# Performance work log

Hardware: AMD Instinct MI355X
Metric: run time of the kernel (lower is better)

The kernel has to match this reference:

```python
import jax, jax.numpy as jnp
import numpy as np

B, S, D_IN, D_EMB = 8, 2048, 512, 512

def setup_inputs() -> dict:
    key = jax.random.key(0)
    ks = jax.random.split(key, 7)
    s = 1.0 / np.sqrt(D_IN)
    return {
        "x": jax.random.normal(ks[0], (B, S, D_IN), dtype=jnp.float32),
        "Wq": jax.random.uniform(ks[1], (D_IN, D_EMB), jnp.float32, -s, s),
        "bq": jax.random.uniform(ks[2], (D_EMB,), jnp.float32, -s, s),
        "Wk": jax.random.uniform(ks[3], (D_IN, D_EMB), jnp.float32, -s, s),
        "bk": jax.random.uniform(ks[4], (D_EMB,), jnp.float32, -s, s),
        "Wv": jax.random.uniform(ks[5], (D_IN, D_EMB), jnp.float32, -s, s),
        "bv": jax.random.uniform(ks[6], (D_EMB,), jnp.float32, -s, s),
    }

def reference(x, Wq, bq, Wk, bk, Wv, bv):
    # single-head attention: softmax(QK^T / sqrt(d)) V
    q = x @ Wq + bq            # [B,S,E]
    k = x @ Wk + bk
    v = x @ Wv + bv
    scores = jnp.einsum('bse,bte->bst', q, k) / jnp.sqrt(jnp.float32(D_EMB))
    attn = jax.nn.softmax(scores, axis=-1)  # [B,S,S]
    return jnp.einsum('bst,bte->bse', attn, v)
```

## Files before the change

kernel.cpp:

```cpp
#include <hip/hip_runtime.h>
#include <stdint.h>


using f32x4 = __attribute__((ext_vector_type(4))) float;
using s16x8 = __attribute__((ext_vector_type(8))) short;
using u16x4 = __attribute__((ext_vector_type(4))) unsigned short;

#define S_LEN 2048
#define EMB   512

#define ASYNC16(g, l)                                                     \
  __builtin_amdgcn_global_load_lds(                                       \
      (const __attribute__((address_space(1))) void*)(g),                 \
      (__attribute__((address_space(3))) void*)(l), 16, 0, 0)

__device__ __forceinline__ unsigned short f2bf(float f) {
  union { float f; unsigned u; } v; v.f = f;
  unsigned r = v.u + 0x7fffu + ((v.u >> 16) & 1u);
  return (unsigned short)(r >> 16);
}

__global__ __launch_bounds__(256) void xconv_kernel(
    const float* __restrict__ x, short* __restrict__ xb) {
  int i = (blockIdx.x * 256 + threadIdx.x) * 8;
  f32x4 a = *(const f32x4*)(x + i);
  f32x4 b = *(const f32x4*)(x + i + 4);
  s16x8 h;
  h[0] = (short)f2bf(a[0]); h[1] = (short)f2bf(a[1]);
  h[2] = (short)f2bf(a[2]); h[3] = (short)f2bf(a[3]);
  h[4] = (short)f2bf(b[0]); h[5] = (short)f2bf(b[1]);
  h[6] = (short)f2bf(b[2]); h[7] = (short)f2bf(b[3]);
  *(s16x8*)(xb + i) = h;
}

__global__ __launch_bounds__(256) void wconv_kernel(
    const float* __restrict__ Wq, const float* __restrict__ Wk,
    const float* __restrict__ Wv, short* __restrict__ Wt) {
  __shared__ float T[64][65];
  int bid = blockIdx.x;
  int mat = bid >> 6;
  int t   = bid & 63;
  int k0  = (t & 7) << 6, n0 = (t >> 3) << 6;
  const float* W = (mat == 0) ? Wq : (mat == 1) ? Wk : Wv;
  int tid = threadIdx.x;
  int rr = tid >> 4, cc = tid & 15;
#pragma unroll
  for (int p = 0; p < 4; ++p) {
    int row = p * 16 + rr;
    f32x4 v = *(const f32x4*)(W + (size_t)(k0 + row) * 512 + n0 + cc * 4);
#pragma unroll
    for (int j = 0; j < 4; ++j) T[row][cc * 4 + j] = v[j];
  }
  __syncthreads();
  short* D = Wt + (size_t)mat * 262144;
#pragma unroll
  for (int p = 0; p < 4; ++p) {
    int nrow = p * 16 + rr;
    u16x4 h;
#pragma unroll
    for (int j = 0; j < 4; ++j) h[j] = f2bf(T[cc * 4 + j][nrow]);
    *(u16x4*)(D + (size_t)(n0 + nrow) * 512 + k0 + cc * 4) = h;
  }
}

__global__ __launch_bounds__(256) void qkv_gemm(
    const short* __restrict__ xb, const short* __restrict__ Wt,
    const float* __restrict__ bq, const float* __restrict__ bk,
    const float* __restrict__ bv,
    short* __restrict__ Qg, short* __restrict__ Kg, short* __restrict__ VTg) {
  __shared__ __align__(16) short As[2][128 * 64];
  __shared__ __align__(16) short Bs[2][128 * 64];
  int gid = blockIdx.x;
  int xcd = gid & 7;
  int s   = gid >> 3;
  int mt_l = s / 12;
  int j    = s - mt_l * 12;
  int mat  = j >> 2;
  int nt   = j & 3;
  int mt   = xcd * 16 + mt_l;
  int m0   = mt << 7, n0 = nt << 7;
  const short* W    = Wt + (size_t)mat * 262144;
  const float* bias = (mat == 0) ? bq : (mat == 1) ? bk : bv;

  int tid = threadIdx.x, lane = tid & 63, wv = tid >> 6;
  int l16 = lane & 15, quad = lane >> 4;
  int wr = (wv & 1) << 6, wc = (wv >> 1) << 6;
  int drow = lane >> 3;
  int dchk = (lane & 7) ^ drow;

  const short* asrc[4];
  const short* bsrc[4];
#pragma unroll
  for (int i = 0; i < 4; ++i) {
    int row = (wv * 4 + i) * 8 + drow;
    asrc[i] = xb + (size_t)(m0 + row) * 512 + dchk * 8;
    bsrc[i] = W  + (size_t)(n0 + row) * 512 + dchk * 8;
  }

  const f32x4 Z4 = {0.f, 0.f, 0.f, 0.f};
  f32x4 acc[4][4];
#pragma unroll
  for (int a = 0; a < 4; ++a)
#pragma unroll
    for (int c = 0; c < 4; ++c) acc[a][c] = Z4;

#pragma unroll
  for (int i = 0; i < 4; ++i) {
    int g = wv * 4 + i;
    ASYNC16(asrc[i], &As[0][g * 512]);
    ASYNC16(bsrc[i], &Bs[0][g * 512]);
  }
  __syncthreads();

  for (int it = 0; it < 8; ++it) {
    int buf = it & 1;
    if (it < 7) {
      int k1 = (it + 1) << 6;
#pragma unroll
      for (int i = 0; i < 4; ++i) {
        int g = wv * 4 + i;
        ASYNC16(asrc[i] + k1, &As[buf ^ 1][g * 512]);
        ASYNC16(bsrc[i] + k1, &Bs[buf ^ 1][g * 512]);
      }
    }
#pragma unroll
    for (int kk = 0; kk < 2; ++kk) {
      s16x8 af[4], bfr[4];
#pragma unroll
      for (int rb = 0; rb < 4; ++rb) {
        int row = wr + rb * 16 + l16;
        int c   = kk * 4 + quad;
        af[rb] = *(const s16x8*)(&As[buf][row * 64 + ((c ^ (row & 7)) * 8)]);
      }
#pragma unroll
      for (int cb = 0; cb < 4; ++cb) {
        int row = wc + cb * 16 + l16;
        int c   = kk * 4 + quad;
        bfr[cb] = *(const s16x8*)(&Bs[buf][row * 64 + ((c ^ (row & 7)) * 8)]);
      }
#pragma unroll
      for (int rb = 0; rb < 4; ++rb)
#pragma unroll
        for (int cb = 0; cb < 4; ++cb)
          acc[rb][cb] = __builtin_amdgcn_mfma_f32_16x16x32_bf16(af[rb], bfr[cb], acc[rb][cb], 0, 0, 0);
    }
    __syncthreads();
  }

  float bsv[4];
#pragma unroll
  for (int cb = 0; cb < 4; ++cb) bsv[cb] = bias[n0 + wc + cb * 16 + l16];

  if (mat < 2) {
    short* D  = (mat == 0) ? Qg : Kg;
    short* Ct = &As[0][0];
#pragma unroll
    for (int rb = 0; rb < 4; ++rb)
#pragma unroll
      for (int cb = 0; cb < 4; ++cb)
#pragma unroll
        for (int r = 0; r < 4; ++r) {
          int m_l = wr + rb * 16 + quad * 4 + r;
          int e_l = wc + cb * 16 + l16;
          int cc  = e_l >> 3;
          Ct[m_l * 128 + ((cc ^ (m_l & 7)) * 8) + (e_l & 7)] =
              (short)f2bf(acc[rb][cb][r] + bsv[cb]);
        }
    __syncthreads();
#pragma unroll
    for (int g = 0; g < 8; ++g) {
      int row = wv * 32 + g * 4 + (lane >> 4);
      int cc  = lane & 15;
      s16x8 v = *(const s16x8*)(Ct + row * 128 + ((cc ^ (row & 7)) * 8));
      *(s16x8*)(D + (size_t)(m0 + row) * 512 + n0 + cc * 8) = v;
    }
  } else {
#pragma unroll
    for (int rb = 0; rb < 4; ++rb)
#pragma unroll
      for (int cb = 0; cb < 4; ++cb) {
        u16x4 h;
#pragma unroll
        for (int r = 0; r < 4; ++r) h[r] = f2bf(acc[rb][cb][r] + bsv[cb]);
        int m  = m0 + wr + rb * 16 + quad * 4;
        int bb = m >> 11, sl = m & 2047;
        int e  = n0 + wc + cb * 16 + l16;
        size_t idx = ((((size_t)bb * 32 + (e >> 4)) * 64 + (sl >> 5)) * 16 +
                      (e & 15)) * 32 + (sl & 31);
        *(u16x4*)(VTg + idx) = h;
      }
  }
}

__global__ __launch_bounds__(512, 2) void attn_kernel(
    const short* __restrict__ Qg, const short* __restrict__ Kg,
    const short* __restrict__ VTg, float* __restrict__ out) {
  __shared__ __align__(16) short Kt[3][32 * 512];
  __shared__ __align__(16) short Pl[2][64 * 40];
  __shared__ float l_l[64];
  const float SCL2 = 0.06375871855f;

  int b = blockIdx.x & 7, qt = blockIdx.x >> 3;
  int s0 = qt << 6;
  int rot = (qt << 1) & 63;
  int tid = threadIdx.x, lane = tid & 63, wv = tid >> 6;
  int l16 = lane & 15, quad = lane >> 4;

  const short* Kb = Kg  + (size_t)b * S_LEN * 512;
  const short* Vb = VTg + (size_t)b * 1048576;

  const short* kdma[4];
#pragma unroll
  for (int i = 0; i < 4; ++i) {
    int r = wv * 4 + i;
    kdma[i] = Kb + (size_t)r * 512 + ((lane ^ (r & 7)) * 8);
  }

  {
    size_t a0 = (size_t)rot * 16384;
    size_t a1 = (size_t)((rot + 1) & 63) * 16384;
#pragma unroll
    for (int i = 0; i < 4; ++i)
      ASYNC16(kdma[i] + a0, &Kt[0][(wv * 4 + i) * 512]);
#pragma unroll
    for (int i = 0; i < 4; ++i)
      ASYNC16(kdma[i] + a1, &Kt[1][(wv * 4 + i) * 512]);
  }

  if (wv < 4) {
    int a = wv & 1, h = wv >> 1;
    const short* qrowA = Qg + ((size_t)b * S_LEN + s0 + a * 32 + l16) * 512 + quad * 8;
    const short* qrowB = qrowA + (size_t)16 * 512;
    s16x8 qfA[16], qfB[16];
#pragma unroll
    for (int c = 0; c < 16; ++c) {
      qfA[c] = *(const s16x8*)(qrowA + c * 32);
      qfB[c] = *(const s16x8*)(qrowB + c * 32);
    }
    const f32x4 Z4 = {0.f, 0.f, 0.f, 0.f};
    f32x4 lsumA = Z4, lsumB = Z4;

    __syncthreads();

    for (int kt = 0; kt < 64; ++kt) {
      int rbuf = kt % 3, wbuf = (kt + 2) % 3;
      {
        size_t adv = (size_t)((kt + 2 + rot) & 63) * 16384;
#pragma unroll
        for (int i = 0; i < 4; ++i)
          ASYNC16(kdma[i] + adv, &Kt[wbuf][(wv * 4 + i) * 512]);
      }
      __builtin_amdgcn_sched_barrier(0);

      f32x4 sA = Z4, sB = Z4;
      int krow = h * 16 + l16;
      const short* kb = &Kt[rbuf][krow * 512];
      int ksw = krow & 7;
      __builtin_amdgcn_s_setprio(1);
#pragma unroll
      for (int c = 0; c < 16; ++c) {
        s16x8 kf = *(const s16x8*)(kb + (((c * 4 + quad) ^ ksw) * 8));
        sA = __builtin_amdgcn_mfma_f32_16x16x32_bf16(qfA[c], kf, sA, 0, 0, 0);
        sB = __builtin_amdgcn_mfma_f32_16x16x32_bf16(qfB[c], kf, sB, 0, 0, 0);
      }
      __builtin_amdgcn_s_setprio(0);

      short* Pc = Pl[kt & 1];
#pragma unroll
      for (int r = 0; r < 4; ++r) {
        float pA = exp2f(sA[r] * SCL2);
        lsumA[r] += pA;
        Pc[(a * 32 + quad * 4 + r) * 40 + h * 16 + l16] = (short)f2bf(pA);
        float pB = exp2f(sB[r] * SCL2);
        lsumB[r] += pB;
        Pc[(a * 32 + 16 + quad * 4 + r) * 40 + h * 16 + l16] = (short)f2bf(pB);
      }

      asm volatile("s_waitcnt vmcnt(4) lgkmcnt(0)\n\ts_barrier" ::: "memory");
      __builtin_amdgcn_sched_barrier(0);
    }

#pragma unroll
    for (int r = 0; r < 4; ++r) {
      float vA = lsumA[r];
      vA += __shfl_xor(vA, 1); vA += __shfl_xor(vA, 2);
      vA += __shfl_xor(vA, 4); vA += __shfl_xor(vA, 8);
      lsumA[r] = vA;
      float vB = lsumB[r];
      vB += __shfl_xor(vB, 1); vB += __shfl_xor(vB, 2);
      vB += __shfl_xor(vB, 4); vB += __shfl_xor(vB, 8);
      lsumB[r] = vB;
    }
    if (h == 0 && l16 == 0) {
#pragma unroll
      for (int r = 0; r < 4; ++r) {
        l_l[a * 32 + quad * 4 + r]      = lsumA[r];
        l_l[a * 32 + 16 + quad * 4 + r] = lsumB[r];
      }
    }
    __syncthreads();
    if (h == 1 && l16 == 0) {
#pragma unroll
      for (int r = 0; r < 4; ++r) {
        l_l[a * 32 + quad * 4 + r]      += lsumA[r];
        l_l[a * 32 + 16 + quad * 4 + r] += lsumB[r];
      }
    }
    __syncthreads();
  } else {
    int pw = wv - 4;
    int e0 = pw << 7;
    const short* vbase = Vb + (size_t)pw * 262144 + l16 * 32 + quad * 8;

    const f32x4 Z4 = {0.f, 0.f, 0.f, 0.f};
    f32x4 acc[4][8];
#pragma unroll
    for (int g = 0; g < 4; ++g)
#pragma unroll
      for (int cb = 0; cb < 8; ++cb) acc[g][cb] = Z4;
    s16x8 vfA[8], vfB[8];

    __syncthreads();

    for (int kt = 0; kt < 64; kt += 2) {
      {
        size_t adv = (size_t)((kt + 2 + rot) & 63) * 16384;
        int wbuf = (kt + 2) % 3;
#pragma unroll
        for (int i = 0; i < 4; ++i)
          ASYNC16(kdma[i] + adv, &Kt[wbuf][(wv * 4 + i) * 512]);
      }
      {
        size_t vadv = (size_t)((kt + rot) & 63) * 512;
#pragma unroll
        for (int cb = 0; cb < 8; ++cb)
          vfA[cb] = *(const s16x8*)(vbase + (size_t)cb * 32768 + vadv);
      }
      if (kt) {
        s16x8 pf[4];
#pragma unroll
        for (int g = 0; g < 4; ++g)
          pf[g] = *(const s16x8*)(&Pl[1][(g * 16 + l16) * 40 + quad * 8]);
        __builtin_amdgcn_s_setprio(1);
#pragma unroll
        for (int cb = 0; cb < 8; ++cb)
#pragma unroll
          for (int g = 0; g < 4; ++g)
            acc[g][cb] = __builtin_amdgcn_mfma_f32_16x16x32_bf16(pf[g], vfB[cb], acc[g][cb], 0, 0, 0);
        __builtin_amdgcn_s_setprio(0);
      }
      asm volatile("s_waitcnt lgkmcnt(0)\n\ts_barrier" ::: "memory");
      __builtin_amdgcn_sched_barrier(0);

      {
        size_t adv = (size_t)((kt + 3 + rot) & 63) * 16384;
        int wbuf = (kt + 3) % 3;
#pragma unroll
        for (int i = 0; i < 4; ++i)
          ASYNC16(kdma[i] + adv, &Kt[wbuf][(wv * 4 + i) * 512]);
      }
      {
        size_t vadv = (size_t)((kt + 1 + rot) & 63) * 512;
#pragma unroll
        for (int cb = 0; cb < 8; ++cb)
          vfB[cb] = *(const s16x8*)(vbase + (size_t)cb * 32768 + vadv);
      }
      {
        s16x8 pf[4];
#pragma unroll
        for (int g = 0; g < 4; ++g)
          pf[g] = *(const s16x8*)(&Pl[0][(g * 16 + l16) * 40 + quad * 8]);
        __builtin_amdgcn_s_setprio(1);
#pragma unroll
        for (int cb = 0; cb < 8; ++cb)
#pragma unroll
          for (int g = 0; g < 4; ++g)
            acc[g][cb] = __builtin_amdgcn_mfma_f32_16x16x32_bf16(pf[g], vfA[cb], acc[g][cb], 0, 0, 0);
        __builtin_amdgcn_s_setprio(0);
      }
      asm volatile("s_waitcnt lgkmcnt(0)\n\ts_barrier" ::: "memory");
      __builtin_amdgcn_sched_barrier(0);
    }

    asm volatile("s_waitcnt vmcnt(0)" ::: "memory");
    __builtin_amdgcn_sched_barrier(0);
    {
      s16x8 pf[4];
#pragma unroll
      for (int g = 0; g < 4; ++g)
        pf[g] = *(const s16x8*)(&Pl[1][(g * 16 + l16) * 40 + quad * 8]);
#pragma unroll
      for (int cb = 0; cb < 8; ++cb)
#pragma unroll
        for (int g = 0; g < 4; ++g)
          acc[g][cb] = __builtin_amdgcn_mfma_f32_16x16x32_bf16(pf[g], vfB[cb], acc[g][cb], 0, 0, 0);
    }
    __syncthreads();
    __syncthreads();

#pragma unroll
    for (int g = 0; g < 4; ++g) {
      f32x4 lv = *(const f32x4*)(l_l + g * 16 + quad * 4);
      f32x4 li;
#pragma unroll
      for (int r = 0; r < 4; ++r) li[r] = 1.0f / lv[r];
#pragma unroll
      for (int cb = 0; cb < 8; ++cb)
#pragma unroll
        for (int r = 0; r < 4; ++r)
          out[((size_t)b * S_LEN + s0 + g * 16 + quad * 4 + r) * 512 + e0 + cb * 16 + l16] =
              acc[g][cb][r] * li[r];
    }
  }
}

extern "C" void kernel_launch(void* const* d_in, const int* in_sizes, int n_in,
                              void* d_out, int out_size, void* d_ws, size_t ws_size,
                              hipStream_t stream) {
  const float* x  = (const float*)d_in[0];
  const float* Wq = (const float*)d_in[1];
  const float* bq = (const float*)d_in[2];
  const float* Wk = (const float*)d_in[3];
  const float* bk = (const float*)d_in[4];
  const float* Wv = (const float*)d_in[5];
  const float* bv = (const float*)d_in[6];

  short* Wt  = (short*)d_ws;
  short* xb  = (short*)((char*)d_ws + 1572864);
  short* Qg  = xb + (size_t)8388608;
  short* Kg  = Qg + (size_t)8388608;
  short* VTg = Kg + (size_t)8388608;

  xconv_kernel<<<4096, 256, 0, stream>>>(x, xb);
  wconv_kernel<<<192, 256, 0, stream>>>(Wq, Wk, Wv, Wt);
  qkv_gemm<<<1536, 256, 0, stream>>>(xb, Wt, bq, bk, bv, Qg, Kg, VTg);
  attn_kernel<<<256, 512, 0, stream>>>(Qg, Kg, VTg, (float*)d_out);
}
```

Before: 213.7 us.

## Merge conversion kernels and fuse QKV GEMM with attention via cooperative grid sync

```diff
diff --git a/kernel.cpp b/kernel.cpp
--- a/kernel.cpp
+++ b/kernel.cpp
@@ -1,5 +1,8 @@
 #include <hip/hip_runtime.h>
+#include <hip/hip_cooperative_groups.h>
 #include <stdint.h>
+
+namespace cg = cooperative_groups;
 
 
 using f32x4 = __attribute__((ext_vector_type(4))) float;
@@ -20,396 +23,413 @@
   return (unsigned short)(r >> 16);
 }
 
-__global__ __launch_bounds__(256) void xconv_kernel(
-    const float* __restrict__ x, short* __restrict__ xb) {
-  int i = (blockIdx.x * 256 + threadIdx.x) * 8;
-  f32x4 a = *(const f32x4*)(x + i);
-  f32x4 b = *(const f32x4*)(x + i + 4);
-  s16x8 h;
-  h[0] = (short)f2bf(a[0]); h[1] = (short)f2bf(a[1]);
-  h[2] = (short)f2bf(a[2]); h[3] = (short)f2bf(a[3]);
-  h[4] = (short)f2bf(b[0]); h[5] = (short)f2bf(b[1]);
-  h[6] = (short)f2bf(b[2]); h[7] = (short)f2bf(b[3]);
-  *(s16x8*)(xb + i) = h;
-}
-
-__global__ __launch_bounds__(256) void wconv_kernel(
+__global__ __launch_bounds__(256) void conv_kernel(
+    const float* __restrict__ x, short* __restrict__ xb,
     const float* __restrict__ Wq, const float* __restrict__ Wk,
     const float* __restrict__ Wv, short* __restrict__ Wt) {
   __shared__ float T[64][65];
-  int bid = blockIdx.x;
-  int mat = bid >> 6;
-  int t   = bid & 63;
-  int k0  = (t & 7) << 6, n0 = (t >> 3) << 6;
-  const float* W = (mat == 0) ? Wq : (mat == 1) ? Wk : Wv;
-  int tid = threadIdx.x;
-  int rr = tid >> 4, cc = tid & 15;
-#pragma unroll
-  for (int p = 0; p < 4; ++p) {
-    int row = p * 16 + rr;
-    f32x4 v = *(const f32x4*)(W + (size_t)(k0 + row) * 512 + n0 + cc * 4);
-#pragma unroll
-    for (int j = 0; j < 4; ++j) T[row][cc * 4 + j] = v[j];
-  }
-  __syncthreads();
-  short* D = Wt + (size_t)mat * 262144;
-#pragma unroll
-  for (int p = 0; p < 4; ++p) {
-    int nrow = p * 16 + rr;
-    u16x4 h;
-#pragma unroll
-    for (int j = 0; j < 4; ++j) h[j] = f2bf(T[cc * 4 + j][nrow]);
-    *(u16x4*)(D + (size_t)(n0 + nrow) * 512 + k0 + cc * 4) = h;
+  if (blockIdx.x < 4096) {
+    int i = (blockIdx.x * 256 + threadIdx.x) * 8;
+    f32x4 a = *(const f32x4*)(x + i);
+    f32x4 b = *(const f32x4*)(x + i + 4);
+    s16x8 h;
+    h[0] = (short)f2bf(a[0]); h[1] = (short)f2bf(a[1]);
+    h[2] = (short)f2bf(a[2]); h[3] = (short)f2bf(a[3]);
+    h[4] = (short)f2bf(b[0]); h[5] = (short)f2bf(b[1]);
+    h[6] = (short)f2bf(b[2]); h[7] = (short)f2bf(b[3]);
+    *(s16x8*)(xb + i) = h;
+  } else {
+    int bid = blockIdx.x - 4096;
+    int mat = bid >> 6;
+    int t   = bid & 63;
+    int k0  = (t & 7) << 6, n0 = (t >> 3) << 6;
+    const float* W = (mat == 0) ? Wq : (mat == 1) ? Wk : Wv;
+    int tid = threadIdx.x;
+    int rr = tid >> 4, cc = tid & 15;
+#pragma unroll
+    for (int p = 0; p < 4; ++p) {
+      int row = p * 16 + rr;
+      f32x4 v = *(const f32x4*)(W + (size_t)(k0 + row) * 512 + n0 + cc * 4);
+#pragma unroll
+      for (int j = 0; j < 4; ++j) T[row][cc * 4 + j] = v[j];
+    }
+    __syncthreads();
+    short* D = Wt + (size_t)mat * 262144;
+#pragma unroll
+    for (int p = 0; p < 4; ++p) {
+      int nrow = p * 16 + rr;
+      u16x4 h;
+#pragma unroll
+      for (int j = 0; j < 4; ++j) h[j] = f2bf(T[cc * 4 + j][nrow]);
+      *(u16x4*)(D + (size_t)(n0 + nrow) * 512 + k0 + cc * 4) = h;
+    }
   }
 }
 
-__global__ __launch_bounds__(256) void qkv_gemm(
+__global__ __launch_bounds__(512, 2) void mega_kernel(
     const short* __restrict__ xb, const short* __restrict__ Wt,
     const float* __restrict__ bq, const float* __restrict__ bk,
     const float* __restrict__ bv,
-    short* __restrict__ Qg, short* __restrict__ Kg, short* __restrict__ VTg) {
-  __shared__ __align__(16) short As[2][128 * 64];
-  __shared__ __align__(16) short Bs[2][128 * 64];
-  int gid = blockIdx.x;
-  int xcd = gid & 7;
-  int s   = gid >> 3;
-  int mt_l = s / 12;
-  int j    = s - mt_l * 12;
-  int mat  = j >> 2;
-  int nt   = j & 3;
-  int mt   = xcd * 16 + mt_l;
-  int m0   = mt << 7, n0 = nt << 7;
-  const short* W    = Wt + (size_t)mat * 262144;
-  const float* bias = (mat == 0) ? bq : (mat == 1) ? bk : bv;
-
-  int tid = threadIdx.x, lane = tid & 63, wv = tid >> 6;
-  int l16 = lane & 15, quad = lane >> 4;
-  int wr = (wv & 1) << 6, wc = (wv >> 1) << 6;
-  int drow = lane >> 3;
-  int dchk = (lane & 7) ^ drow;
-
-  const short* asrc[4];
-  const short* bsrc[4];
-#pragma unroll
-  for (int i = 0; i < 4; ++i) {
-    int row = (wv * 4 + i) * 8 + drow;
-    asrc[i] = xb + (size_t)(m0 + row) * 512 + dchk * 8;
-    bsrc[i] = W  + (size_t)(n0 + row) * 512 + dchk * 8;
-  }
-
-  const f32x4 Z4 = {0.f, 0.f, 0.f, 0.f};
-  f32x4 acc[4][4];
-#pragma unroll
-  for (int a = 0; a < 4; ++a)
-#pragma unroll
-    for (int c = 0; c < 4; ++c) acc[a][c] = Z4;
-
-#pragma unroll
-  for (int i = 0; i < 4; ++i) {
-    int g = wv * 4 + i;
-    ASYNC16(asrc[i], &As[0][g * 512]);
-    ASYNC16(bsrc[i], &Bs[0][g * 512]);
-  }
-  __syncthreads();
-
-  for (int it = 0; it < 8; ++it) {
-    int buf = it & 1;
-    if (it < 7) {
-      int k1 = (it + 1) << 6;
+    short* __restrict__ Qg, short* __restrict__ Kg, short* __restrict__ VTg,
+    float* __restrict__ out) {
+  __shared__ __align__(16) char SM[131072];
+  const float SCL2 = 0.06375871855f;
+
+  int blk = blockIdx.x, tid = threadIdx.x;
+  int lane512 = tid & 63;
+
+  {
+    int hh = tid >> 8;
+    int tl = tid & 255;
+    int lane = tl & 63, wv = tl >> 6;
+    int l16 = lane & 15, quad = lane >> 4;
+    int xcd = blk & 7;
+
+    short* As = (short*)(SM + hh * 65536);
+    short* Bs = (short*)(SM + hh * 65536 + 32768);
+
+    int wr = (wv & 1) << 6, wc = (wv >> 1) << 6;
+    int drow = lane >> 3;
+    int dchk = (lane & 7) ^ drow;
+    const f32x4 Z4 = {0.f, 0.f, 0.f, 0.f};
+
+    for (int job = 0; job < 3; ++job) {
+      int s    = (blk >> 3) * 6 + hh * 3 + job;
+      int mt_l = s / 12;
+      int jj   = s - mt_l * 12;
+      int mat  = jj >> 2;
+      int nt   = jj & 3;
+      int mt   = xcd * 16 + mt_l;
+      int m0   = mt << 7, n0 = nt << 7;
+      const short* W    = Wt + (size_t)mat * 262144;
+      const float* bias = (mat == 0) ? bq : (mat == 1) ? bk : bv;
+
+      const short* asrc[4];
+      const short* bsrc[4];
+#pragma unroll
+      for (int i = 0; i < 4; ++i) {
+        int row = (wv * 4 + i) * 8 + drow;
+        asrc[i] = xb + (size_t)(m0 + row) * 512 + dchk * 8;
+        bsrc[i] = W  + (size_t)(n0 + row) * 512 + dchk * 8;
+      }
+
+      f32x4 acc[4][4];
+#pragma unroll
+      for (int a = 0; a < 4; ++a)
+#pragma unroll
+        for (int c = 0; c < 4; ++c) acc[a][c] = Z4;
+
 #pragma unroll
       for (int i = 0; i < 4; ++i) {
         int g = wv * 4 + i;
-        ASYNC16(asrc[i] + k1, &As[buf ^ 1][g * 512]);
-        ASYNC16(bsrc[i] + k1, &Bs[buf ^ 1][g * 512]);
-      }
-    }
-#pragma unroll
-    for (int kk = 0; kk < 2; ++kk) {
-      s16x8 af[4], bfr[4];
-#pragma unroll
-      for (int rb = 0; rb < 4; ++rb) {
-        int row = wr + rb * 16 + l16;
-        int c   = kk * 4 + quad;
-        af[rb] = *(const s16x8*)(&As[buf][row * 64 + ((c ^ (row & 7)) * 8)]);
-      }
-#pragma unroll
-      for (int cb = 0; cb < 4; ++cb) {
-        int row = wc + cb * 16 + l16;
-        int c   = kk * 4 + quad;
-        bfr[cb] = *(const s16x8*)(&Bs[buf][row * 64 + ((c ^ (row & 7)) * 8)]);
-      }
-#pragma unroll
-      for (int rb = 0; rb < 4; ++rb)
-#pragma unroll
-        for (int cb = 0; cb < 4; ++cb)
-          acc[rb][cb] = __builtin_amdgcn_mfma_f32_16x16x32_bf16(af[rb], bfr[cb], acc[rb][cb], 0, 0, 0);
-    }
-    __syncthreads();
+        ASYNC16(asrc[i], As + g * 512);
+        ASYNC16(bsrc[i], Bs + g * 512);
+      }
+      __syncthreads();
+
+      for (int it = 0; it < 8; ++it) {
+        int buf = it & 1;
+        if (it < 7) {
+          int k1 = (it + 1) << 6;
+#pragma unroll
+          for (int i = 0; i < 4; ++i) {
+            int g = wv * 4 + i;
+            ASYNC16(asrc[i] + k1, As + (buf ^ 1) * 8192 + g * 512);
+            ASYNC16(bsrc[i] + k1, Bs + (buf ^ 1) * 8192 + g * 512);
+          }
+        }
+#pragma unroll
+        for (int kk = 0; kk < 2; ++kk) {
+          s16x8 af[4], bfr[4];
+#pragma unroll
+          for (int rb = 0; rb < 4; ++rb) {
+            int row = wr + rb * 16 + l16;
+            int c   = kk * 4 + quad;
+            af[rb] = *(const s16x8*)(As + buf * 8192 + row * 64 + ((c ^ (row & 7)) * 8));
+          }
+#pragma unroll
+          for (int cb = 0; cb < 4; ++cb) {
+            int row = wc + cb * 16 + l16;
+            int c   = kk * 4 + quad;
+            bfr[cb] = *(const s16x8*)(Bs + buf * 8192 + row * 64 + ((c ^ (row & 7)) * 8));
+          }
+#pragma unroll
+          for (int rb = 0; rb < 4; ++rb)
+#pragma unroll
+            for (int cb = 0; cb < 4; ++cb)
+              acc[rb][cb] = __builtin_amdgcn_mfma_f32_16x16x32_bf16(af[rb], bfr[cb], acc[rb][cb], 0, 0, 0);
+        }
+        __syncthreads();
+      }
+
+      float bsv[4];
+#pragma unroll
+      for (int cb = 0; cb < 4; ++cb) bsv[cb] = bias[n0 + wc + cb * 16 + l16];
+
+      if (mat < 2) {
+        short* D  = (mat == 0) ? Qg : Kg;
+        short* Ct = As;
+#pragma unroll
+        for (int rb = 0; rb < 4; ++rb)
+#pragma unroll
+          for (int cb = 0; cb < 4; ++cb)
+#pragma unroll
+            for (int r = 0; r < 4; ++r) {
+              int m_l = wr + rb * 16 + quad * 4 + r;
+              int e_l = wc + cb * 16 + l16;
+              int cc  = e_l >> 3;
+              Ct[m_l * 128 + ((cc ^ (m_l & 7)) * 8) + (e_l & 7)] =
+                  (short)f2bf(acc[rb][cb][r] + bsv[cb]);
+            }
+        __syncthreads();
+#pragma unroll
+        for (int g = 0; g < 8; ++g) {
+          int row = wv * 32 + g * 4 + (lane >> 4);
+          int cc  = lane & 15;
+          s16x8 v = *(const s16x8*)(Ct + row * 128 + ((cc ^ (row & 7)) * 8));
+          *(s16x8*)(D + (size_t)(m0 + row) * 512 + n0 + cc * 8) = v;
+        }
+        __syncthreads();
+      } else {
+#pragma unroll
+        for (int rb = 0; rb < 4; ++rb)
+#pragma unroll
+          for (int cb = 0; cb < 4; ++cb) {
+            u16x4 h;
+#pragma unroll
+            for (int r = 0; r < 4; ++r) h[r] = f2bf(acc[rb][cb][r] + bsv[cb]);
+            int m  = m0 + wr + rb * 16 + quad * 4;
+            int bb = m >> 11, sl = m & 2047;
+            int e  = n0 + wc + cb * 16 + l16;
+            size_t idx = ((((size_t)bb * 32 + (e >> 4)) * 64 + (sl >> 5)) * 16 +
+                          (e & 15)) * 32 + (sl & 31);
+            *(u16x4*)(VTg + idx) = h;
+          }
+        __syncthreads();
+        __syncthreads();
+      }
+    }
   }
 
-  float bsv[4];
-#pragma unroll
-  for (int cb = 0; cb < 4; ++cb) bsv[cb] = bias[n0 + wc + cb * 16 + l16];
-
-  if (mat < 2) {
-    short* D  = (mat == 0) ? Qg : Kg;
-    short* Ct = &As[0][0];
-#pragma unroll
-    for (int rb = 0; rb < 4; ++rb)
-#pragma unroll
-      for (int cb = 0; cb < 4; ++cb)
+  __threadfence();
+  cg::this_grid().sync();
+
+  {
+    short* Kt  = (short*)SM;
+    short* PlB = (short*)(SM + 98304);
+    float* l_l = (float*)(SM + 98304 + 10240);
+
+    int b = blk & 7, qt = blk >> 3;
+    int s0 = qt << 6;
+    int rot = (qt << 1) & 63;
+    int lane = lane512, wv = tid >> 6;
+    int l16 = lane & 15, quad = lane >> 4;
+
+    const short* Kb = Kg  + (size_t)b * S_LEN * 512;
+    const short* Vb = VTg + (size_t)b * 1048576;
+
+    const short* kdma[4];
+#pragma unroll
+    for (int i = 0; i < 4; ++i) {
+      int r = wv * 4 + i;
+      kdma[i] = Kb + (size_t)r * 512 + ((lane ^ (r & 7)) * 8);
+    }
+
+    {
+      size_t a0 = (size_t)rot * 16384;
+      size_t a1 = (size_t)((rot + 1) & 63) * 16384;
+#pragma unroll
+      for (int i = 0; i < 4; ++i)
+        ASYNC16(kdma[i] + a0, Kt + (wv * 4 + i) * 512);
+#pragma unroll
+      for (int i = 0; i < 4; ++i)
+        ASYNC16(kdma[i] + a1, Kt + 16384 + (wv * 4 + i) * 512);
+    }
+
+    if (wv < 4) {
+      int a = wv & 1, h = wv >> 1;
+      const short* qrowA = Qg + ((size_t)b * S_LEN + s0 + a * 32 + l16) * 512 + quad * 8;
+      const short* qrowB = qrowA + (size_t)16 * 512;
+      s16x8 qfA[16], qfB[16];
+#pragma unroll
+      for (int c = 0; c < 16; ++c) {
+        qfA[c] = *(const s16x8*)(qrowA + c * 32);
+        qfB[c] = *(const s16x8*)(qrowB + c * 32);
+      }
+      const f32x4 Z4 = {0.f, 0.f, 0.f, 0.f};
+      f32x4 lsumA = Z4, lsumB = Z4;
+
+      __syncthreads();
+
+      for (int kt = 0; kt < 64; ++kt) {
+        int rbuf = kt % 3, wbuf = (kt + 2) % 3;
+        {
+          size_t adv = (size_t)((kt + 2 + rot) & 63) * 16384;
+#pragma unroll
+          for (int i = 0; i < 4; ++i)
+            ASYNC16(kdma[i] + adv, Kt + wbuf * 16384 + (wv * 4 + i) * 512);
+        }
+        __builtin_amdgcn_sched_barrier(0);
+
+        f32x4 sA = Z4, sB = Z4;
+        int krow = h * 16 + l16;
+        const short* kb = Kt + rbuf * 16384 + krow * 512;
+        int ksw = krow & 7;
+        __builtin_amdgcn_s_setprio(1);
+#pragma unroll
+        for (int c = 0; c < 16; ++c) {
+          s16x8 kf = *(const s16x8*)(kb + (((c * 4 + quad) ^ ksw) * 8));
+          sA = __builtin_amdgcn_mfma_f32_16x16x32_bf16(qfA[c], kf, sA, 0, 0, 0);
+          sB = __builtin_amdgcn_mfma_f32_16x16x32_bf16(qfB[c], kf, sB, 0, 0, 0);
+        }
+        __builtin_amdgcn_s_setprio(0);
+
+        short* Pc = PlB + (kt & 1) * 2560;
 #pragma unroll
         for (int r = 0; r < 4; ++r) {
-          int m_l = wr + rb * 16 + quad * 4 + r;
-          int e_l = wc + cb * 16 + l16;
-          int cc  = e_l >> 3;
-          Ct[m_l * 128 + ((cc ^ (m_l & 7)) * 8) + (e_l & 7)] =
-              (short)f2bf(acc[rb][cb][r] + bsv[cb]);
-        }
-    __syncthreads();
-#pragma unroll
-    for (int g = 0; g < 8; ++g) {
-      int row = wv * 32 + g * 4 + (lane >> 4);
-      int cc  = lane & 15;
-      s16x8 v = *(const s16x8*)(Ct + row * 128 + ((cc ^ (row & 7)) * 8));
-      *(s16x8*)(D + (size_t)(m0 + row) * 512 + n0 + cc * 8) = v;
-    }
-  } else {
-#pragma unroll
-    for (int rb = 0; rb < 4; ++rb)
-#pragma unroll
-      for (int cb = 0; cb < 4; ++cb) {
-        u16x4 h;
-#pragma unroll
-        for (int r = 0; r < 4; ++r) h[r] = f2bf(acc[rb][cb][r] + bsv[cb]);
-        int m  = m0 + wr + rb * 16 + quad * 4;
-        int bb = m >> 11, sl = m & 2047;
-        int e  = n0 + wc + cb * 16 + l16;
-        size_t idx = ((((size_t)bb * 32 + (e >> 4)) * 64 + (sl >> 5)) * 16 +
-                      (e & 15)) * 32 + (sl & 31);
-        *(u16x4*)(VTg + idx) = h;
-      }
-  }
-}
-
-__global__ __launch_bounds__(512, 2) void attn_kernel(
-    const short* __restrict__ Qg, const short* __restrict__ Kg,
-    const short* __restrict__ VTg, float* __restrict__ out) {
-  __shared__ __align__(16) short Kt[3][32 * 512];
-  __shared__ __align__(16) short Pl[2][64 * 40];
-  __shared__ float l_l[64];
-  const float SCL2 = 0.06375871855f;
-
-  int b = blockIdx.x & 7, qt = blockIdx.x >> 3;
-  int s0 = qt << 6;
-  int rot = (qt << 1) & 63;
-  int tid = threadIdx.x, lane = tid & 63, wv = tid >> 6;
-  int l16 = lane & 15, quad = lane >> 4;
-
-  const short* Kb = Kg  + (size_t)b * S_LEN * 512;
-  const short* Vb = VTg + (size_t)b * 1048576;
-
-  const short* kdma[4];
-#pragma unroll
-  for (int i = 0; i < 4; ++i) {
-    int r = wv * 4 + i;
-    kdma[i] = Kb + (size_t)r * 512 + ((lane ^ (r & 7)) * 8);
-  }
-
-  {
-    size_t a0 = (size_t)rot * 16384;
-    size_t a1 = (size_t)((rot + 1) & 63) * 16384;
-#pragma unroll
-    for (int i = 0; i < 4; ++i)
-      ASYNC16(kdma[i] + a0, &Kt[0][(wv * 4 + i) * 512]);
-#pragma unroll
-    for (int i = 0; i < 4; ++i)
-      ASYNC16(kdma[i] + a1, &Kt[1][(wv * 4 + i) * 512]);
-  }
-
-  if (wv < 4) {
-    int a = wv & 1, h = wv >> 1;
-    const short* qrowA = Qg + ((size_t)b * S_LEN + s0 + a * 32 + l16) * 512 + quad * 8;
-    const short* qrowB = qrowA + (size_t)16 * 512;
-    s16x8 qfA[16], qfB[16];
-#pragma unroll
-    for (int c = 0; c < 16; ++c) {
-      qfA[c] = *(const s16x8*)(qrowA + c * 32);
-      qfB[c] = *(const s16x8*)(qrowB + c * 32);
-    }
-    const f32x4 Z4 = {0.f, 0.f, 0.f, 0.f};
-    f32x4 lsumA = Z4, lsumB = Z4;
-
-    __syncthreads();
-
-    for (int kt = 0; kt < 64; ++kt) {
-      int rbuf = kt % 3, wbuf = (kt + 2) % 3;
+          float pA = exp2f(sA[r] * SCL2);
+          lsumA[r] += pA;
+          Pc[(a * 32 + quad * 4 + r) * 40 + h * 16 + l16] = (short)f2bf(pA);
+          float pB = exp2f(sB[r] * SCL2);
+          lsumB[r] += pB;
+          Pc[(a * 32 + 16 + quad * 4 + r) * 40 + h * 16 + l16] = (short)f2bf(pB);
+        }
+
+        asm volatile("s_waitcnt vmcnt(4) lgkmcnt(0)\n\ts_barrier" ::: "memory");
+        __builtin_amdgcn_sched_barrier(0);
+      }
+
+#pragma unroll
+      for (int r = 0; r < 4; ++r) {
+        float vA = lsumA[r];
+        vA += __shfl_xor(vA, 1); vA += __shfl_xor(vA, 2);
+        vA += __shfl_xor(vA, 4); vA += __shfl_xor(vA, 8);
+        lsumA[r] = vA;
+        float vB = lsumB[r];
+        vB += __shfl_xor(vB, 1); vB += __shfl_xor(vB, 2);
+        vB += __shfl_xor(vB, 4); vB += __shfl_xor(vB, 8);
+        lsumB[r] = vB;
+      }
+      if (h == 0 && l16 == 0) {
+#pragma unroll
+        for (int r = 0; r < 4; ++r) {
+          l_l[a * 32 + quad * 4 + r]      = lsumA[r];
+          l_l[a * 32 + 16 + quad * 4 + r] = lsumB[r];
+        }
+      }
+      __syncthreads();
+      if (h == 1 && l16 == 0) {
+#pragma unroll
+        for (int r = 0; r < 4; ++r) {
+          l_l[a * 32 + quad * 4 + r]      += lsumA[r];
+          l_l[a * 32 + 16 + quad * 4 + r] += lsumB[r];
+        }
+      }
+      __syncthreads();
+    } else {
+      int pw = wv - 4;
+      int e0 = pw << 7;
+      const short* vbase = Vb + (size_t)pw * 262144 + l16 * 32 + quad * 8;
+
+      const f32x4 Z4 = {0.f, 0.f, 0.f, 0.f};
+      f32x4 acc[4][8];
+#pragma unroll
+      for (int g = 0; g < 4; ++g)
+#pragma unroll
+        for (int cb = 0; cb < 8; ++cb) acc[g][cb] = Z4;
+      s16x8 vfA[8], vfB[8];
+
+      __syncthreads();
+
+      for (int kt = 0; kt < 64; kt += 2) {
+        {
+          size_t adv = (size_t)((kt + 2 + rot) & 63) * 16384;
+          int wbuf = (kt + 2) % 3;
+#pragma unroll
+          for (int i = 0; i < 4; ++i)
+            ASYNC16(kdma[i] + adv, Kt + wbuf * 16384 + (wv * 4 + i) * 512);
+        }
+        {
+          size_t vadv = (size_t)((kt + rot) & 63) * 512;
+#pragma unroll
+          for (int cb = 0; cb < 8; ++cb)
+            vfA[cb] = *(const s16x8*)(vbase + (size_t)cb * 32768 + vadv);
+        }
+        if (kt) {
+          s16x8 pf[4];
+#pragma unroll
+          for (int g = 0; g < 4; ++g)
+            pf[g] = *(const s16x8*)(PlB + 2560 + (g * 16 + l16) * 40 + quad * 8);
+          __builtin_amdgcn_s_setprio(1);
+#pragma unroll
+          for (int cb = 0; cb < 8; ++cb)
+#pragma unroll
+            for (int g = 0; g < 4; ++g)
+              acc[g][cb] = __builtin_amdgcn_mfma_f32_16x16x32_bf16(pf[g], vfB[cb], acc[g][cb], 0, 0, 0);
+          __builtin_amdgcn_s_setprio(0);
+        }
+        asm volatile("s_waitcnt lgkmcnt(0)\n\ts_barrier" ::: "memory");
+        __builtin_amdgcn_sched_barrier(0);
+
+        {
+          size_t adv = (size_t)((kt + 3 + rot) & 63) * 16384;
+          int wbuf = (kt + 3) % 3;
+#pragma unroll
+          for (int i = 0; i < 4; ++i)
+            ASYNC16(kdma[i] + adv, Kt + wbuf * 16384 + (wv * 4 + i) * 512);
+        }
+        {
+          size_t vadv = (size_t)((kt + 1 + rot) & 63) * 512;
+#pragma unroll
+          for (int cb = 0; cb < 8; ++cb)
+            vfB[cb] = *(const s16x8*)(vbase + (size_t)cb * 32768 + vadv);
+        }
+        {
+          s16x8 pf[4];
+#pragma unroll
+          for (int g = 0; g < 4; ++g)
+            pf[g] = *(const s16x8*)(PlB + (g * 16 + l16) * 40 + quad * 8);
+          __builtin_amdgcn_s_setprio(1);
+#pragma unroll
+          for (int cb = 0; cb < 8; ++cb)
+#pragma unroll
+            for (int g = 0; g < 4; ++g)
+              acc[g][cb] = __builtin_amdgcn_mfma_f32_16x16x32_bf16(pf[g], vfA[cb], acc[g][cb], 0, 0, 0);
+          __builtin_amdgcn_s_setprio(0);
+        }
+        asm volatile("s_waitcnt lgkmcnt(0)\n\ts_barrier" ::: "memory");
+        __builtin_amdgcn_sched_barrier(0);
+      }
+
+      asm volatile("s_waitcnt vmcnt(0)" ::: "memory");
+      __builtin_amdgcn_sched_barrier(0);
       {
-        size_t adv = (size_t)((kt + 2 + rot) & 63) * 16384;
-#pragma unroll
-        for (int i = 0; i < 4; ++i)
-          ASYNC16(kdma[i] + adv, &Kt[wbuf][(wv * 4 + i) * 512]);
-      }
-      __builtin_amdgcn_sched_barrier(0);
-
-      f32x4 sA = Z4, sB = Z4;
-      int krow = h * 16 + l16;
-      const short* kb = &Kt[rbuf][krow * 512];
-      int ksw = krow & 7;
-      __builtin_amdgcn_s_setprio(1);
-#pragma unroll
-      for (int c = 0; c < 16; ++c) {
-        s16x8 kf = *(const s16x8*)(kb + (((c * 4 + quad) ^ ksw) * 8));
-        sA = __builtin_amdgcn_mfma_f32_16x16x32_bf16(qfA[c], kf, sA, 0, 0, 0);
-        sB = __builtin_amdgcn_mfma_f32_16x16x32_bf16(qfB[c], kf, sB, 0, 0, 0);
-      }
-      __builtin_amdgcn_s_setprio(0);
-
-      short* Pc = Pl[kt & 1];
-#pragma unroll
-      for (int r = 0; r < 4; ++r) {
-        float pA = exp2f(sA[r] * SCL2);
-        lsumA[r] += pA;
-        Pc[(a * 32 + quad * 4 + r) * 40 + h * 16 + l16] = (short)f2bf(pA);
-        float pB = exp2f(sB[r] * SCL2);
-        lsumB[r] += pB;
-        Pc[(a * 32 + 16 + quad * 4 + r) * 40 + h * 16 + l16] = (short)f2bf(pB);
-      }
-
-      asm volatile("s_waitcnt vmcnt(4) lgkmcnt(0)\n\ts_barrier" ::: "memory");
-      __builtin_amdgcn_sched_barrier(0);
-    }
-
-#pragma unroll
-    for (int r = 0; r < 4; ++r) {
-      float vA = lsumA[r];
-      vA += __shfl_xor(vA, 1); vA += __shfl_xor(vA, 2);
-      vA += __shfl_xor(vA, 4); vA += __shfl_xor(vA, 8);
-      lsumA[r] = vA;
-      float vB = lsumB[r];
-      vB += __shfl_xor(vB, 1); vB += __shfl_xor(vB, 2);
-      vB += __shfl_xor(vB, 4); vB += __shfl_xor(vB, 8);
-      lsumB[r] = vB;
-    }
-    if (h == 0 && l16 == 0) {
-#pragma unroll
-      for (int r = 0; r < 4; ++r) {
-        l_l[a * 32 + quad * 4 + r]      = lsumA[r];
-        l_l[a * 32 + 16 + quad * 4 + r] = lsumB[r];
-      }
-    }
-    __syncthreads();
-    if (h == 1 && l16 == 0) {
-#pragma unroll
-      for (int r = 0; r < 4; ++r) {
-        l_l[a * 32 + quad * 4 + r]      += lsumA[r];
-        l_l[a * 32 + 16 + quad * 4 + r] += lsumB[r];
-      }
-    }
-    __syncthreads();
-  } else {
-    int pw = wv - 4;
-    int e0 = pw << 7;
-    const short* vbase = Vb + (size_t)pw * 262144 + l16 * 32 + quad * 8;
-
-    const f32x4 Z4 = {0.f, 0.f, 0.f, 0.f};
-    f32x4 acc[4][8];
-#pragma unroll
-    for (int g = 0; g < 4; ++g)
-#pragma unroll
-      for (int cb = 0; cb < 8; ++cb) acc[g][cb] = Z4;
-    s16x8 vfA[8], vfB[8];
-
-    __syncthreads();
-
-    for (int kt = 0; kt < 64; kt += 2) {
-      {
-        size_t adv = (size_t)((kt + 2 + rot) & 63) * 16384;
-        int wbuf = (kt + 2) % 3;
-#pragma unroll
-        for (int i = 0; i < 4; ++i)
-          ASYNC16(kdma[i] + adv, &Kt[wbuf][(wv * 4 + i) * 512]);
-      }
-      {
-        size_t vadv = (size_t)((kt + rot) & 63) * 512;
-#pragma unroll
-        for (int cb = 0; cb < 8; ++cb)
-          vfA[cb] = *(const s16x8*)(vbase + (size_t)cb * 32768 + vadv);
-      }
-      if (kt) {
         s16x8 pf[4];
 #pragma unroll
         for (int g = 0; g < 4; ++g)
-          pf[g] = *(const s16x8*)(&Pl[1][(g * 16 + l16) * 40 + quad * 8]);
-        __builtin_amdgcn_s_setprio(1);
+          pf[g] = *(const s16x8*)(PlB + 2560 + (g * 16 + l16) * 40 + quad * 8);
 #pragma unroll
         for (int cb = 0; cb < 8; ++cb)
 #pragma unroll
           for (int g = 0; g < 4; ++g)
             acc[g][cb] = __builtin_amdgcn_mfma_f32_16x16x32_bf16(pf[g], vfB[cb], acc[g][cb], 0, 0, 0);
-        __builtin_amdgcn_s_setprio(0);
-      }
-      asm volatile("s_waitcnt lgkmcnt(0)\n\ts_barrier" ::: "memory");
-      __builtin_amdgcn_sched_barrier(0);
-
-      {
-        size_t adv = (size_t)((kt + 3 + rot) & 63) * 16384;
-        int wbuf = (kt + 3) % 3;
-#pragma unroll
-        for (int i = 0; i < 4; ++i)
-          ASYNC16(kdma[i] + adv, &Kt[wbuf][(wv * 4 + i) * 512]);
-      }
-      {
-        size_t vadv = (size_t)((kt + 1 + rot) & 63) * 512;
+      }
+      __syncthreads();
+      __syncthreads();
+
+#pragma unroll
+      for (int g = 0; g < 4; ++g) {
+        f32x4 lv = *(const f32x4*)(l_l + g * 16 + quad * 4);
+        f32x4 li;
+#pragma unroll
+        for (int r = 0; r < 4; ++r) li[r] = 1.0f / lv[r];
 #pragma unroll
         for (int cb = 0; cb < 8; ++cb)
-          vfB[cb] = *(const s16x8*)(vbase + (size_t)cb * 32768 + vadv);
-      }
-      {
-        s16x8 pf[4];
-#pragma unroll
-        for (int g = 0; g < 4; ++g)
-          pf[g] = *(const s16x8*)(&Pl[0][(g * 16 + l16) * 40 + quad * 8]);
-        __builtin_amdgcn_s_setprio(1);
-#pragma unroll
-        for (int cb = 0; cb < 8; ++cb)
-#pragma unroll
-          for (int g = 0; g < 4; ++g)
-            acc[g][cb] = __builtin_amdgcn_mfma_f32_16x16x32_bf16(pf[g], vfA[cb], acc[g][cb], 0, 0, 0);
-        __builtin_amdgcn_s_setprio(0);
-      }
-      asm volatile("s_waitcnt lgkmcnt(0)\n\ts_barrier" ::: "memory");
-      __builtin_amdgcn_sched_barrier(0);
-    }
-
-    asm volatile("s_waitcnt vmcnt(0)" ::: "memory");
-    __builtin_amdgcn_sched_barrier(0);
-    {
-      s16x8 pf[4];
-#pragma unroll
-      for (int g = 0; g < 4; ++g)
-        pf[g] = *(const s16x8*)(&Pl[1][(g * 16 + l16) * 40 + quad * 8]);
-#pragma unroll
-      for (int cb = 0; cb < 8; ++cb)
-#pragma unroll
-        for (int g = 0; g < 4; ++g)
-          acc[g][cb] = __builtin_amdgcn_mfma_f32_16x16x32_bf16(pf[g], vfB[cb], acc[g][cb], 0, 0, 0);
-    }
-    __syncthreads();
-    __syncthreads();
-
-#pragma unroll
-    for (int g = 0; g < 4; ++g) {
-      f32x4 lv = *(const f32x4*)(l_l + g * 16 + quad * 4);
-      f32x4 li;
-#pragma unroll
-      for (int r = 0; r < 4; ++r) li[r] = 1.0f / lv[r];
-#pragma unroll
-      for (int cb = 0; cb < 8; ++cb)
-#pragma unroll
-        for (int r = 0; r < 4; ++r)
-          out[((size_t)b * S_LEN + s0 + g * 16 + quad * 4 + r) * 512 + e0 + cb * 16 + l16] =
-              acc[g][cb][r] * li[r];
+#pragma unroll
+          for (int r = 0; r < 4; ++r)
+            out[((size_t)b * S_LEN + s0 + g * 16 + quad * 4 + r) * 512 + e0 + cb * 16 + l16] =
+                acc[g][cb][r] * li[r];
+      }
     }
   }
 }
@@ -430,9 +450,12 @@
   short* Qg  = xb + (size_t)8388608;
   short* Kg  = Qg + (size_t)8388608;
   short* VTg = Kg + (size_t)8388608;
-
-  xconv_kernel<<<4096, 256, 0, stream>>>(x, xb);
-  wconv_kernel<<<192, 256, 0, stream>>>(Wq, Wk, Wv, Wt);
-  qkv_gemm<<<1536, 256, 0, stream>>>(xb, Wt, bq, bk, bv, Qg, Kg, VTg);
-  attn_kernel<<<256, 512, 0, stream>>>(Qg, Kg, VTg, (float*)d_out);
+  float* outp = (float*)d_out;
+
+  conv_kernel<<<4288, 256, 0, stream>>>(x, xb, Wq, Wk, Wv, Wt);
+
+  void* args[] = {(void*)&xb, (void*)&Wt, (void*)&bq, (void*)&bk, (void*)&bv,
+                  (void*)&Qg, (void*)&Kg, (void*)&VTg, (void*)&outp};
+  hipLaunchCooperativeKernel((void*)mega_kernel, dim3(256), dim3(512),
+                             args, 0, stream);
 }
```

Measured after the change: 307.2 us. +43.7%, slower.

## Fuse Q and K projections per block to share the x tile

Applied to the files above, without the earlier changes.

```diff
diff --git a/kernel.cpp b/kernel.cpp
--- a/kernel.cpp
+++ b/kernel.cpp
@@ -68,113 +68,210 @@
     const float* __restrict__ bq, const float* __restrict__ bk,
     const float* __restrict__ bv,
     short* __restrict__ Qg, short* __restrict__ Kg, short* __restrict__ VTg) {
-  __shared__ __align__(16) short As[2][128 * 64];
-  __shared__ __align__(16) short Bs[2][128 * 64];
+  __shared__ __align__(16) char SM[65536];
   int gid = blockIdx.x;
   int xcd = gid & 7;
   int s   = gid >> 3;
-  int mt_l = s / 12;
-  int j    = s - mt_l * 12;
-  int mat  = j >> 2;
-  int nt   = j & 3;
-  int mt   = xcd * 16 + mt_l;
-  int m0   = mt << 7, n0 = nt << 7;
-  const short* W    = Wt + (size_t)mat * 262144;
-  const float* bias = (mat == 0) ? bq : (mat == 1) ? bk : bv;
-
   int tid = threadIdx.x, lane = tid & 63, wv = tid >> 6;
   int l16 = lane & 15, quad = lane >> 4;
   int wr = (wv & 1) << 6, wc = (wv >> 1) << 6;
-  int drow = lane >> 3;
-  int dchk = (lane & 7) ^ drow;
-
-  const short* asrc[4];
-  const short* bsrc[4];
-#pragma unroll
-  for (int i = 0; i < 4; ++i) {
-    int row = (wv * 4 + i) * 8 + drow;
-    asrc[i] = xb + (size_t)(m0 + row) * 512 + dchk * 8;
-    bsrc[i] = W  + (size_t)(n0 + row) * 512 + dchk * 8;
-  }
-
   const f32x4 Z4 = {0.f, 0.f, 0.f, 0.f};
-  f32x4 acc[4][4];
-#pragma unroll
-  for (int a = 0; a < 4; ++a)
-#pragma unroll
-    for (int c = 0; c < 4; ++c) acc[a][c] = Z4;
-
-#pragma unroll
-  for (int i = 0; i < 4; ++i) {
-    int g = wv * 4 + i;
-    ASYNC16(asrc[i], &As[0][g * 512]);
-    ASYNC16(bsrc[i], &Bs[0][g * 512]);
-  }
-  __syncthreads();
-
-  for (int it = 0; it < 8; ++it) {
-    int buf = it & 1;
-    if (it < 7) {
-      int k1 = (it + 1) << 6;
-#pragma unroll
-      for (int i = 0; i < 4; ++i) {
-        int g = wv * 4 + i;
-        ASYNC16(asrc[i] + k1, &As[buf ^ 1][g * 512]);
-        ASYNC16(bsrc[i] + k1, &Bs[buf ^ 1][g * 512]);
-      }
-    }
-#pragma unroll
-    for (int kk = 0; kk < 2; ++kk) {
-      s16x8 af[4], bfr[4];
+
+  if (s < 64) {
+    int mt_l = s >> 2, nt = s & 3;
+    int mt = xcd * 16 + mt_l;
+    int m0 = mt << 7, n0 = nt << 7;
+    short* Asm = (short*)SM;
+    short* Bqs = (short*)(SM + 16384);
+    short* Bks = (short*)(SM + 32768);
+
+    int drow = lane >> 2;
+    int dchk = (lane & 3) ^ (drow & 3);
+    const short* asrc[2];
+    const short* bqsrc[2];
+    const short* bksrc[2];
+#pragma unroll
+    for (int i = 0; i < 2; ++i) {
+      int row = (wv * 2 + i) * 16 + drow;
+      asrc[i]  = xb + (size_t)(m0 + row) * 512 + dchk * 8;
+      bqsrc[i] = Wt + (size_t)(n0 + row) * 512 + dchk * 8;
+      bksrc[i] = Wt + 262144 + (size_t)(n0 + row) * 512 + dchk * 8;
+    }
+
+    f32x4 accQ[4][4], accK[4][4];
+#pragma unroll
+    for (int a = 0; a < 4; ++a)
+#pragma unroll
+      for (int c = 0; c < 4; ++c) { accQ[a][c] = Z4; accK[a][c] = Z4; }
+
+#pragma unroll
+    for (int i = 0; i < 2; ++i) {
+      int g = wv * 2 + i;
+      ASYNC16(asrc[i],  Asm + g * 512);
+      ASYNC16(bqsrc[i], Bqs + g * 512);
+      ASYNC16(bksrc[i], Bks + g * 512);
+    }
+    __syncthreads();
+
+    for (int it = 0; it < 16; ++it) {
+      int buf = it & 1;
+      if (it < 15) {
+        int k1 = (it + 1) << 5;
+#pragma unroll
+        for (int i = 0; i < 2; ++i) {
+          int g = wv * 2 + i;
+          ASYNC16(asrc[i] + k1,  Asm + (buf ^ 1) * 4096 + g * 512);
+          ASYNC16(bqsrc[i] + k1, Bqs + (buf ^ 1) * 4096 + g * 512);
+          ASYNC16(bksrc[i] + k1, Bks + (buf ^ 1) * 4096 + g * 512);
+        }
+      }
+      s16x8 af[4], bqf[4], bkf[4];
 #pragma unroll
       for (int rb = 0; rb < 4; ++rb) {
         int row = wr + rb * 16 + l16;
-        int c   = kk * 4 + quad;
-        af[rb] = *(const s16x8*)(&As[buf][row * 64 + ((c ^ (row & 7)) * 8)]);
+        af[rb] = *(const s16x8*)(Asm + buf * 4096 + row * 32 + ((quad ^ (row & 3)) * 8));
       }
 #pragma unroll
       for (int cb = 0; cb < 4; ++cb) {
         int row = wc + cb * 16 + l16;
-        int c   = kk * 4 + quad;
-        bfr[cb] = *(const s16x8*)(&Bs[buf][row * 64 + ((c ^ (row & 7)) * 8)]);
+        int off = buf * 4096 + row * 32 + ((quad ^ (row & 3)) * 8);
+        bqf[cb] = *(const s16x8*)(Bqs + off);
+        bkf[cb] = *(const s16x8*)(Bks + off);
       }
 #pragma unroll
       for (int rb = 0; rb < 4; ++rb)
 #pragma unroll
+        for (int cb = 0; cb < 4; ++cb) {
+          accQ[rb][cb] = __builtin_amdgcn_mfma_f32_16x16x32_bf16(af[rb], bqf[cb], accQ[rb][cb], 0, 0, 0);
+          accK[rb][cb] = __builtin_amdgcn_mfma_f32_16x16x32_bf16(af[rb], bkf[cb], accK[rb][cb], 0, 0, 0);
+        }
+      __syncthreads();
+    }
+
+    short* Ct = (short*)SM;
+    {
+      float bsv[4];
+#pragma unroll
+      for (int cb = 0; cb < 4; ++cb) bsv[cb] = bq[n0 + wc + cb * 16 + l16];
+#pragma unroll
+      for (int rb = 0; rb < 4; ++rb)
+#pragma unroll
         for (int cb = 0; cb < 4; ++cb)
-          acc[rb][cb] = __builtin_amdgcn_mfma_f32_16x16x32_bf16(af[rb], bfr[cb], acc[rb][cb], 0, 0, 0);
-    }
-    __syncthreads();
-  }
-
-  float bsv[4];
-#pragma unroll
-  for (int cb = 0; cb < 4; ++cb) bsv[cb] = bias[n0 + wc + cb * 16 + l16];
-
-  if (mat < 2) {
-    short* D  = (mat == 0) ? Qg : Kg;
-    short* Ct = &As[0][0];
-#pragma unroll
-    for (int rb = 0; rb < 4; ++rb)
-#pragma unroll
-      for (int cb = 0; cb < 4; ++cb)
-#pragma unroll
-        for (int r = 0; r < 4; ++r) {
-          int m_l = wr + rb * 16 + quad * 4 + r;
-          int e_l = wc + cb * 16 + l16;
-          int cc  = e_l >> 3;
-          Ct[m_l * 128 + ((cc ^ (m_l & 7)) * 8) + (e_l & 7)] =
-              (short)f2bf(acc[rb][cb][r] + bsv[cb]);
+#pragma unroll
+          for (int r = 0; r < 4; ++r) {
+            int m_l = wr + rb * 16 + quad * 4 + r;
+            int e_l = wc + cb * 16 + l16;
+            int cc  = e_l >> 3;
+            Ct[m_l * 128 + ((cc ^ (m_l & 7)) * 8) + (e_l & 7)] =
+                (short)f2bf(accQ[rb][cb][r] + bsv[cb]);
+          }
+      __syncthreads();
+#pragma unroll
+      for (int g = 0; g < 8; ++g) {
+        int row = wv * 32 + g * 4 + (lane >> 4);
+        int cc  = lane & 15;
+        s16x8 v = *(const s16x8*)(Ct + row * 128 + ((cc ^ (row & 7)) * 8));
+        *(s16x8*)(Qg + (size_t)(m0 + row) * 512 + n0 + cc * 8) = v;
+      }
+      __syncthreads();
+    }
+    {
+      float bsv[4];
+#pragma unroll
+      for (int cb = 0; cb < 4; ++cb) bsv[cb] = bk[n0 + wc + cb * 16 + l16];
+#pragma unroll
+      for (int rb = 0; rb < 4; ++rb)
+#pragma unroll
+        for (int cb = 0; cb < 4; ++cb)
+#pragma unroll
+          for (int r = 0; r < 4; ++r) {
+            int m_l = wr + rb * 16 + quad * 4 + r;
+            int e_l = wc + cb * 16 + l16;
+            int cc  = e_l >> 3;
+            Ct[m_l * 128 + ((cc ^ (m_l & 7)) * 8) + (e_l & 7)] =
+                (short)f2bf(accK[rb][cb][r] + bsv[cb]);
+          }
+      __syncthreads();
+#pragma unroll
+      for (int g = 0; g < 8; ++g) {
+        int row = wv * 32 + g * 4 + (lane >> 4);
+        int cc  = lane & 15;
+        s16x8 v = *(const s16x8*)(Ct + row * 128 + ((cc ^ (row & 7)) * 8));
+        *(s16x8*)(Kg + (size_t)(m0 + row) * 512 + n0 + cc * 8) = v;
+      }
+    }
+  } else {
+    int s2 = s - 64;
+    int mt_l = s2 >> 2, nt = s2 & 3;
+    int mt = xcd * 16 + mt_l;
+    int m0 = mt << 7, n0 = nt << 7;
+    const short* W = Wt + (size_t)2 * 262144;
+    short* As = (short*)SM;
+    short* Bs = (short*)(SM + 32768);
+
+    int drow = lane >> 3;
+    int dchk = (lane & 7) ^ drow;
+    const short* asrc[4];
+    const short* bsrc[4];
+#pragma unroll
+    for (int i = 0; i < 4; ++i) {
+      int row = (wv * 4 + i) * 8 + drow;
+      asrc[i] = xb + (size_t)(m0 + row) * 512 + dchk * 8;
+      bsrc[i] = W  + (size_t)(n0 + row) * 512 + dchk * 8;
+    }
+
+    f32x4 acc[4][4];
+#pragma unroll
+    for (int a = 0; a < 4; ++a)
+#pragma unroll
+      for (int c = 0; c < 4; ++c) acc[a][c] = Z4;
+
+#pragma unroll
+    for (int i = 0; i < 4; ++i) {
+      int g = wv * 4 + i;
+      ASYNC16(asrc[i], As + g * 512);
+      ASYNC16(bsrc[i], Bs + g * 512);
+    }
+    __syncthreads();
+
+    for (int it = 0; it < 8; ++it) {
+      int buf = it & 1;
+      if (it < 7) {
+        int k1 = (it + 1) << 6;
+#pragma unroll
+        for (int i = 0; i < 4; ++i) {
+          int g = wv * 4 + i;
+          ASYNC16(asrc[i] + k1, As + (buf ^ 1) * 8192 + g * 512);
+          ASYNC16(bsrc[i] + k1, Bs + (buf ^ 1) * 8192 + g * 512);
         }
-    __syncthreads();
-#pragma unroll
-    for (int g = 0; g < 8; ++g) {
-      int row = wv * 32 + g * 4 + (lane >> 4);
-      int cc  = lane & 15;
-      s16x8 v = *(const s16x8*)(Ct + row * 128 + ((cc ^ (row & 7)) * 8));
-      *(s16x8*)(D + (size_t)(m0 + row) * 512 + n0 + cc * 8) = v;
-    }
-  } else {
+      }
+#pragma unroll
+      for (int kk = 0; kk < 2; ++kk) {
+        s16x8 af[4], bfr[4];
+#pragma unroll
+        for (int rb = 0; rb < 4; ++rb) {
+          int row = wr + rb * 16 + l16;
+          int c   = kk * 4 + quad;
+          af[rb] = *(const s16x8*)(As + buf * 8192 + row * 64 + ((c ^ (row & 7)) * 8));
+        }
+#pragma unroll
+        for (int cb = 0; cb < 4; ++cb) {
+          int row = wc + cb * 16 + l16;
+          int c   = kk * 4 + quad;
+          bfr[cb] = *(const s16x8*)(Bs + buf * 8192 + row * 64 + ((c ^ (row & 7)) * 8));
+        }
+#pragma unroll
+        for (int rb = 0; rb < 4; ++rb)
+#pragma unroll
+          for (int cb = 0; cb < 4; ++cb)
+            acc[rb][cb] = __builtin_amdgcn_mfma_f32_16x16x32_bf16(af[rb], bfr[cb], acc[rb][cb], 0, 0, 0);
+      }
+      __syncthreads();
+    }
+
+    float bsv[4];
+#pragma unroll
+    for (int cb = 0; cb < 4; ++cb) bsv[cb] = bv[n0 + wc + cb * 16 + l16];
 #pragma unroll
     for (int rb = 0; rb < 4; ++rb)
 #pragma unroll
@@ -433,6 +530,6 @@
 
   xconv_kernel<<<4096, 256, 0, stream>>>(x, xb);
   wconv_kernel<<<192, 256, 0, stream>>>(Wq, Wk, Wv, Wt);
-  qkv_gemm<<<1536, 256, 0, stream>>>(xb, Wt, bq, bk, bv, Qg, Kg, VTg);
+  qkv_gemm<<<1024, 256, 0, stream>>>(xb, Wt, bq, bk, bv, Qg, Kg, VTg);
   attn_kernel<<<256, 512, 0, stream>>>(Qg, Kg, VTg, (float*)d_out);
 }
```

Result: slower. 224.8 us (+5.2%).
